# Performance work log

Hardware: AMD Instinct MI355X
Metric: run time of the kernel (lower is better)

The kernel has to match this reference:

```python
import jax, jax.numpy as jnp
import numpy as np

N_ATOMS = 65536
N_PAIRS = N_ATOMS * 32
MAXZ = 95          # D3 tables cover H..Pu, indexed directly by atomic number
NREF = 5           # number of reference coordination numbers per element
CUTOFF, CUTON = 12.0, 10.0   # model units; distances_model2Bohr == 1
K1, K3 = 16.0, -4.0
SMALL = 1e-30      # fp32 stand-in for the original's 1e-300 double guard


def setup_inputs() -> dict:
    key = jax.random.key(0)
    k0, k1, k2, k3 = jax.random.split(key, 4)
    rng = np.random.default_rng(0)

    atomic_numbers = jax.random.randint(k0, (N_ATOMS,), 1, 87)
    idx_i = jax.random.randint(k1, (N_PAIRS,), 0, N_ATOMS)
    idx_j = jax.random.randint(k2, (N_PAIRS,), 0, N_ATOMS)
    # pair distances spanning inside/switch/outside of the 10..12 cutoff band
    distances = jax.random.uniform(k3, (N_PAIRS,), minval=0.8, maxval=12.5)

    # synthetic stand-ins for the grimme_d3 data files
    rcov = jnp.asarray(rng.uniform(0.5, 3.0, (MAXZ,)).astype(np.float32))
    rcn_np = rng.uniform(0.0, 5.0, (MAXZ, NREF)).astype(np.float32)
    rcn_np[::3, NREF - 1] = -1.0  # mimic -1 padding for missing references
    rcn = jnp.asarray(rcn_np)
    rc6 = jnp.asarray(rng.uniform(1.0, 50.0, (MAXZ, MAXZ, NREF, NREF)).astype(np.float32))
    r2r4 = jnp.asarray(rng.uniform(1.0, 10.0, (MAXZ,)).astype(np.float32))

    s6 = jnp.float32(1.0)
    s8 = jnp.float32(0.9171)
    a1 = jnp.float32(0.3385)
    a2 = jnp.float32(2.883)
    return dict(distances=distances, rcov=rcov, rcn=rcn, rc6=rc6, r2r4=r2r4,
                s6=s6, s8=s8, a1=a1, a2=a2,
                atomic_numbers=atomic_numbers, idx_i=idx_i, idx_j=idx_j)


def reference(distances, rcov, rcn, rc6, r2r4, s6, s8, a1, a2,
              atomic_numbers, idx_i, idx_j):
    n = atomic_numbers.shape[0]
    zi = atomic_numbers[idx_i]
    zj = atomic_numbers[idx_j]

    # smooth switch-off from 1 (r < cuton) to 0 (r >= cutoff)
    x = (CUTOFF - distances) / (CUTOFF - CUTON)
    sw = jnp.where(distances < CUTON, 1.0,
                   jnp.where(distances >= CUTOFF, 0.0,
                             ((6.0 * x - 15.0) * x + 10.0) * x * x * x))

    # coordination numbers via inverse damping, scatter-summed per atom i
    rcov_ij = rcov[zi] + rcov[zj]
    cn_ij = sw / (1.0 + jnp.exp(-K1 * (rcov_ij / distances - 1.0)))
    cn = jax.ops.segment_sum(cn_ij, idx_i, num_segments=n)  # [N]

    # Gaussian weights over reference CNs (soft retrieval into rc6 table)
    rcn_a = rcn[atomic_numbers]                 # [N, NREF]
    mask = rcn_a >= 0
    dcn = rcn_a - cn[:, None]
    gw = jnp.where(mask, jnp.exp(K3 * dcn * dcn), 0.0)
    norm = jnp.sum(gw, axis=-1, keepdims=True)
    # exceptional case: all gaussians underflow -> pick the max reference CN
    rcn_max_a = jnp.max(rcn, axis=-1)[atomic_numbers][:, None]
    exceptional = (rcn_a == rcn_max_a).astype(gw.dtype)
    weights = jnp.where(norm == 0, exceptional, gw / jnp.maximum(norm, SMALL))  # [N, NREF]

    # weighted pairwise C6 from reference table rc6[Zi, Zj, a, b]
    w_i = weights[idx_i]                         # [P, NREF]
    w_j = weights[idx_j]                         # [P, NREF]
    c6 = jnp.einsum('pa,pb,pab->p', w_i, w_j, rc6[zi, zj])

    # C8 = 3 * C6 * <r2>/<r4>_i * <r2>/<r4>_j ; BJ critical radius
    qq = 3.0 * r2r4[zi] * r2r4[zj]
    rr = a1 * jnp.sqrt(qq) + a2

    d2 = distances * distances
    d6 = d2 * d2 * d2
    d8 = d6 * d2
    rr2 = rr * rr
    rr6 = rr2 * rr2 * rr2
    rr8 = rr6 * rr2

    # BJ-damped dispersion energy per pair (0.5 for double counting), switched
    e_pair = -0.5 * (s6 * c6 / (d6 + rr6) + s8 * qq * c6 / (d8 + rr8)) * sw

    # per-atom dispersion energies (energies_Hartree2model == 1)
    return jax.ops.segment_sum(e_pair, idx_i, num_segments=n)
```

## Files before the change

kernel.cpp:

```cpp
#include <hip/hip_runtime.h>
#include <stdint.h>


typedef unsigned short u16;
#define MAXZ 95
#define NREF 5
#define EXC_CUT -87.33654f
#define NB    1024
#define BSH   6
#define BSZ   64
#define CAPSH 12
#define RC_TOTAL (MAXZ * MAXZ * 32)

__device__ __forceinline__ float switch_fn(float d) {
    if (d < 10.0f) return 1.0f;
    float x = (12.0f - d) * 0.5f;
    return ((6.0f * x - 15.0f) * x + 10.0f) * x * x * x;
}

__device__ __forceinline__ void calc_weights(const float* __restrict__ rcn_z,
                                             float cni, float* __restrict__ w) {
    float r[NREF], arg[NREF];
    float rmax = -1e30f, marg = -1e30f;
#pragma unroll
    for (int a = 0; a < NREF; a++) {
        r[a] = rcn_z[a];
        rmax = fmaxf(rmax, r[a]);
        float dc = r[a] - cni;
        arg[a] = (-4.0f * dc) * dc;
        if (r[a] >= 0.0f) marg = fmaxf(marg, arg[a]);
    }
    if (marg < EXC_CUT) {
#pragma unroll
        for (int a = 0; a < NREF; a++) w[a] = (r[a] == rmax) ? 1.0f : 0.0f;
    } else {
        float g[NREF], norm = 0.0f;
#pragma unroll
        for (int a = 0; a < NREF; a++) {
            float e = (r[a] >= 0.0f) ? expf(arg[a]) : 0.0f;
            g[a] = e;
            norm += e;
        }
        float inv = 1.0f / fmaxf(norm, 1e-30f);
#pragma unroll
        for (int a = 0; a < NREF; a++) w[a] = g[a] * inv;
    }
}

__global__ __launch_bounds__(1024) void scatter_pairs(const float* __restrict__ dist,
                                                      const int* __restrict__ idx_i,
                                                      const int* __restrict__ idx_j,
                                                      const int* __restrict__ Z,
                                                      const float* __restrict__ rcov,
                                                      const float* __restrict__ rc6,
                                                      float* __restrict__ rcovA,
                                                      float* __restrict__ rc6pad,
                                                      uint32_t* __restrict__ bcount,
                                                      uint2* __restrict__ recs,
                                                      int n_pairs, int n_atoms,
                                                      int chunk) {
    __shared__ uint32_t hist[NB];
    __shared__ uint32_t run[NB];

    int g = blockIdx.x * 1024 + (int)threadIdx.x;
    int T = gridDim.x * 1024;
    for (int i = g; i < n_atoms; i += T) rcovA[i] = rcov[Z[i]];
    for (int id = g; id < RC_TOTAL; id += T) {
        int tile = id >> 5, slot = id & 31;
        rc6pad[id] = (slot < 25) ? rc6[(size_t)tile * 25 + slot] : 0.0f;
    }

    for (int t = threadIdx.x; t < NB; t += 1024) hist[t] = 0;
    __syncthreads();
    int lo = blockIdx.x * chunk;
    int hi = min(lo + chunk, n_pairs);
    for (int q = lo + (int)threadIdx.x; q < hi; q += 1024) {
        if (dist[q] < 12.0f)
            atomicAdd(&hist[((uint32_t)idx_i[q]) >> BSH], 1u);
    }
    __syncthreads();
    for (int t = threadIdx.x; t < NB; t += 1024) {
        uint32_t h = hist[t];
        run[t] = h ? atomicAdd(&bcount[t], h) : 0u;
    }
    __syncthreads();
    for (int q = lo + (int)threadIdx.x; q < hi; q += 1024) {
        float d = dist[q];
        if (d >= 12.0f) continue;
        uint32_t i = (uint32_t)idx_i[q];
        uint32_t b = i >> BSH;
        uint32_t pos = atomicAdd(&run[b], 1u);
        if (pos < (1u << CAPSH)) {
            uint32_t packed = ((uint32_t)idx_j[q] & 0xFFFFu) |
                              ((i & (BSZ - 1u)) << 16);
            recs[((size_t)b << CAPSH) + pos] = make_uint2(__float_as_uint(d), packed);
        }
    }
}

__global__ __launch_bounds__(256) void cn_bucket(const uint2* __restrict__ recs,
                                                 const uint32_t* __restrict__ bcount,
                                                 const float* __restrict__ rcovA,
                                                 float* __restrict__ cn,
                                                 int n_atoms) {
    __shared__ float lrc[BSZ];
    __shared__ float acc[BSZ];
    int b = blockIdx.x;
    int base = b << BSH;
    if (threadIdx.x < BSZ) {
        int i = base + (int)threadIdx.x;
        lrc[threadIdx.x] = (i < n_atoms) ? rcovA[i] : 0.0f;
        acc[threadIdx.x] = 0.0f;
    }
    __syncthreads();
    uint32_t n = min(bcount[b], 1u << CAPSH);
    const uint2* r0 = recs + ((size_t)b << CAPSH);
    for (uint32_t k = threadIdx.x; k < n; k += 256) {
        uint2 r = r0[k];
        float d = __uint_as_float(r.x);
        int j  = r.y & 0xFFFF;
        int il = r.y >> 16;
        float rij = lrc[il] + rcovA[j];
        float sw = switch_fn(d);
        atomicAdd(&acc[il], sw / (1.0f + expf(-16.0f * (rij / d - 1.0f))));
    }
    __syncthreads();
    if (threadIdx.x < BSZ) {
        int i = base + (int)threadIdx.x;
        if (i < n_atoms) cn[i] = acc[threadIdx.x];
    }
}

__global__ __launch_bounds__(256) void atom_weights(const float* __restrict__ rcn,
                                                    const float* __restrict__ r2r4,
                                                    const int* __restrict__ Z,
                                                    const float* __restrict__ cn,
                                                    float* __restrict__ arec,
                                                    int n_atoms) {
    int i = blockIdx.x * blockDim.x + threadIdx.x;
    if (i >= n_atoms) return;
    int z = Z[i];
    float w[NREF];
    calc_weights(rcn + (size_t)z * NREF, cn[i], w);
    float4 v0 = make_float4(w[0], w[1], w[2], w[3]);
    float4 v1 = make_float4(w[4], r2r4[z], __int_as_float(z), 0.0f);
    float4* dst = (float4*)(arec + (size_t)i * 8);
    dst[0] = v0;
    dst[1] = v1;
}

__global__ __launch_bounds__(256) void energy_bucket(const uint2* __restrict__ recs,
                                                     const uint32_t* __restrict__ bcount,
                                                     const float* __restrict__ arec,
                                                     const float* __restrict__ rc6pad,
                                                     const float* __restrict__ s6p,
                                                     const float* __restrict__ s8p,
                                                     const float* __restrict__ a1p,
                                                     const float* __restrict__ a2p,
                                                     float* __restrict__ eout,
                                                     int n_atoms) {
    __shared__ float4 la0[BSZ];
    __shared__ float4 la1[BSZ];
    __shared__ float  acc[BSZ];
    int b = blockIdx.x;
    int base = b << BSH;
    if (threadIdx.x < BSZ) {
        int i = min(base + (int)threadIdx.x, n_atoms - 1);
        const float4* A = (const float4*)(arec + (size_t)i * 8);
        la0[threadIdx.x] = A[0];
        la1[threadIdx.x] = A[1];
        acc[threadIdx.x] = 0.0f;
    }
    __syncthreads();
    float s6 = s6p[0], s8 = s8p[0], a1 = a1p[0], a2 = a2p[0];
    uint32_t n = min(bcount[b], 1u << CAPSH);
    const uint2* r0 = recs + ((size_t)b << CAPSH);
    for (uint32_t k = threadIdx.x; k < n; k += 256) {
        uint2 r = r0[k];
        float d = __uint_as_float(r.x);
        int j  = r.y & 0xFFFF;
        int il = r.y >> 16;
        float4 ai0 = la0[il];
        float4 ai1 = la1[il];
        const float4* Aj = (const float4*)(arec + (size_t)j * 8);
        float4 aj0 = Aj[0];
        float4 aj1 = Aj[1];
        float wi[NREF] = {ai0.x, ai0.y, ai0.z, ai0.w, ai1.x};
        float wj[NREF] = {aj0.x, aj0.y, aj0.z, aj0.w, aj1.x};
        int zi = __float_as_int(ai1.z);
        int zj = __float_as_int(aj1.z);

        const float4* T4 = (const float4*)(rc6pad + (size_t)(zi * MAXZ + zj) * 32);
        float tt[25];
#pragma unroll
        for (int kk = 0; kk < 6; kk++) {
            float4 t = T4[kk];
            tt[4 * kk + 0] = t.x;
            if (4 * kk + 1 < 25) tt[4 * kk + 1] = t.y;
            if (4 * kk + 2 < 25) tt[4 * kk + 2] = t.z;
            if (4 * kk + 3 < 25) tt[4 * kk + 3] = t.w;
        }
        tt[24] = ((const float*)T4)[24];

        float c6 = 0.0f;
#pragma unroll
        for (int a = 0; a < NREF; a++) {
            float s = 0.0f;
#pragma unroll
            for (int bb = 0; bb < NREF; bb++) s = fmaf(wj[bb], tt[a * NREF + bb], s);
            c6 = fmaf(wi[a], s, c6);
        }

        float qq = 3.0f * ai1.y * aj1.y;
        float rr = a1 * sqrtf(qq) + a2;
        float d2 = d * d;
        float d6 = d2 * d2 * d2;
        float d8 = d6 * d2;
        float rr2 = rr * rr;
        float rr6 = rr2 * rr2 * rr2;
        float rr8 = rr6 * rr2;
        float sw = switch_fn(d);

        float e = -0.5f * (s6 * c6 / (d6 + rr6) + s8 * qq * c6 / (d8 + rr8)) * sw;
        atomicAdd(&acc[il], e);
    }
    __syncthreads();
    if (threadIdx.x < BSZ) {
        int i = base + (int)threadIdx.x;
        if (i < n_atoms) eout[i] = acc[threadIdx.x];
    }
}

__global__ __launch_bounds__(256) void pair_cn_slim(const float* __restrict__ dist,
                                                    const float* __restrict__ rcov,
                                                    const int* __restrict__ Z,
                                                    const int* __restrict__ idx_i,
                                                    const int* __restrict__ idx_j,
                                                    float* __restrict__ cn,
                                                    int n_pairs) {
    int p = blockIdx.x * blockDim.x + threadIdx.x;
    if (p >= n_pairs) return;
    float d = dist[p];
    if (d >= 12.0f) return;
    float rij = rcov[Z[idx_i[p]]] + rcov[Z[idx_j[p]]];
    float sw = switch_fn(d);
    atomicAdd(&cn[idx_i[p]], sw / (1.0f + expf(-16.0f * (rij / d - 1.0f))));
}

__global__ __launch_bounds__(256) void pair_energy_slim(const float* __restrict__ dist,
                                                        const int* __restrict__ Z,
                                                        const int* __restrict__ idx_i,
                                                        const int* __restrict__ idx_j,
                                                        const float* __restrict__ cn,
                                                        const float* __restrict__ rcn,
                                                        const float* __restrict__ r2r4,
                                                        const float* __restrict__ rc6,
                                                        const float* __restrict__ s6p,
                                                        const float* __restrict__ s8p,
                                                        const float* __restrict__ a1p,
                                                        const float* __restrict__ a2p,
                                                        float* __restrict__ eout,
                                                        int n_pairs) {
    int p = blockIdx.x * blockDim.x + threadIdx.x;
    if (p >= n_pairs) return;
    float d = dist[p];
    if (d >= 12.0f) return;
    int i = idx_i[p], j = idx_j[p];
    int zi = Z[i], zj = Z[j];
    float wi[NREF], wj[NREF];
    calc_weights(rcn + (size_t)zi * NREF, cn[i], wi);
    calc_weights(rcn + (size_t)zj * NREF, cn[j], wj);
    const float* T = rc6 + (size_t)(zi * MAXZ + zj) * 25;
    float c6 = 0.0f;
#pragma unroll
    for (int a = 0; a < NREF; a++) {
        float s = 0.0f;
#pragma unroll
        for (int bb = 0; bb < NREF; bb++) s = fmaf(wj[bb], T[a * NREF + bb], s);
        c6 = fmaf(wi[a], s, c6);
    }
    float qq = 3.0f * r2r4[zi] * r2r4[zj];
    float rr = a1p[0] * sqrtf(qq) + a2p[0];
    float d2 = d * d;
    float d6 = d2 * d2 * d2;
    float d8 = d6 * d2;
    float rr2 = rr * rr;
    float rr6 = rr2 * rr2 * rr2;
    float rr8 = rr6 * rr2;
    float sw = switch_fn(d);
    float e = -0.5f * (s6p[0] * c6 / (d6 + rr6) + s8p[0] * qq * c6 / (d8 + rr8)) * sw;
    atomicAdd(&eout[i], e);
}

extern "C" void kernel_launch(void* const* d_in, const int* in_sizes, int n_in,
                              void* d_out, int out_size, void* d_ws, size_t ws_size,
                              hipStream_t stream) {
    const float* dist = (const float*)d_in[0];
    const float* rcov = (const float*)d_in[1];
    const float* rcn  = (const float*)d_in[2];
    const float* rc6  = (const float*)d_in[3];
    const float* r2r4 = (const float*)d_in[4];
    const float* s6p  = (const float*)d_in[5];
    const float* s8p  = (const float*)d_in[6];
    const float* a1p  = (const float*)d_in[7];
    const float* a2p  = (const float*)d_in[8];
    const int* Z    = (const int*)d_in[9];
    const int* idxi = (const int*)d_in[10];
    const int* idxj = (const int*)d_in[11];
    float* out = (float*)d_out;

    int n_pairs = in_sizes[0];
    int n_atoms = in_sizes[9];
    int agrid = (n_atoms + 255) / 256;

    char* ws = (char*)d_ws;
    size_t o_bcount = 0;
    size_t o_cn     = (size_t)NB * 4;
    size_t o_rcovA  = o_cn + (size_t)n_atoms * 4;
    size_t o_arec   = (o_rcovA + (size_t)n_atoms * 4 + 31) & ~(size_t)31;
    size_t o_rc6    = o_arec + (size_t)n_atoms * 32;
    size_t o_recs   = (o_rc6 + (size_t)RC_TOTAL * 4 + 255) & ~(size_t)255;
    size_t need     = o_recs + ((size_t)NB << CAPSH) * 8;

    uint32_t* bcount = (uint32_t*)(ws + o_bcount);
    float* cn     = (float*)(ws + o_cn);
    float* rcovA  = (float*)(ws + o_rcovA);
    float* arec   = (float*)(ws + o_arec);
    float* rcpad  = (float*)(ws + o_rc6);
    uint2* recs   = (uint2*)(ws + o_recs);

    if (ws_size >= need && n_atoms <= NB * BSZ) {
        hipMemsetAsync(bcount, 0, NB * 4, stream);
        int sblocks = 256;
        int chunk = (n_pairs + sblocks - 1) / sblocks;
        scatter_pairs<<<sblocks, 1024, 0, stream>>>(dist, idxi, idxj, Z, rcov, rc6,
                                                    rcovA, rcpad, bcount, recs,
                                                    n_pairs, n_atoms, chunk);
        cn_bucket<<<NB, 256, 0, stream>>>(recs, bcount, rcovA, cn, n_atoms);
        atom_weights<<<agrid, 256, 0, stream>>>(rcn, r2r4, Z, cn, arec, n_atoms);
        energy_bucket<<<NB, 256, 0, stream>>>(recs, bcount, arec, rcpad,
                                              s6p, s8p, a1p, a2p, out, n_atoms);
    } else {
        int pgrid = (n_pairs + 255) / 256;
        hipMemsetAsync(out, 0, (size_t)n_atoms * 4, stream);
        hipMemsetAsync(cn, 0, (size_t)n_atoms * 4, stream);
        pair_cn_slim<<<pgrid, 256, 0, stream>>>(dist, rcov, Z, idxi, idxj, cn, n_pairs);
        pair_energy_slim<<<pgrid, 256, 0, stream>>>(dist, Z, idxi, idxj, cn, rcn, r2r4,
                                                    rc6, s6p, s8p, a1p, a2p, out, n_pairs);
    }
}
```

Measured before the change: 172.0 us.

## Pack atom weights and C6 table as fp16, fuse weights into CN kernel

Stores the padded rc6 reference table and the per-atom records (weights, r2r4, Z) in half precision, which halves the bytes fetched per pair in the energy kernel's random gathers. It also computes the per-atom weights directly at the end of the CN bucket kernel, removing the separate atom_weights launch and the cn round trip through memory. The cost is fp16 rounding of the C6 values, weights and r2r4, which may push results past the accuracy tolerance.

```diff
diff --git a/kernel.cpp b/kernel.cpp
--- a/kernel.cpp
+++ b/kernel.cpp
@@ -12,6 +12,13 @@
 #define CAPSH 12
 #define RC_TOTAL (MAXZ * MAXZ * 32)
 
+__device__ __forceinline__ float h2f(u16 h) {
+    union { _Float16 h; u16 u; } v; v.u = h; return (float)v.h;
+}
+__device__ __forceinline__ u16 f2h(float f) {
+    union { _Float16 h; u16 u; } v; v.h = (_Float16)f; return v.u;
+}
+
 __device__ __forceinline__ float switch_fn(float d) {
     if (d < 10.0f) return 1.0f;
     float x = (12.0f - d) * 0.5f;
@@ -45,6 +52,13 @@
 #pragma unroll
         for (int a = 0; a < NREF; a++) w[a] = g[a] * inv;
     }
+}
+
+__device__ __forceinline__ void dec8(uint4 t, float* o) {
+    o[0] = h2f(t.x & 0xFFFFu); o[1] = h2f(t.x >> 16);
+    o[2] = h2f(t.y & 0xFFFFu); o[3] = h2f(t.y >> 16);
+    o[4] = h2f(t.z & 0xFFFFu); o[5] = h2f(t.z >> 16);
+    o[6] = h2f(t.w & 0xFFFFu); o[7] = h2f(t.w >> 16);
 }
 
 __global__ __launch_bounds__(1024) void scatter_pairs(const float* __restrict__ dist,
@@ -54,7 +68,7 @@
                                                       const float* __restrict__ rcov,
                                                       const float* __restrict__ rc6,
                                                       float* __restrict__ rcovA,
-                                                      float* __restrict__ rc6pad,
+                                                      u16* __restrict__ rc6pad,
                                                       uint32_t* __restrict__ bcount,
                                                       uint2* __restrict__ recs,
                                                       int n_pairs, int n_atoms,
@@ -67,7 +81,7 @@
     for (int i = g; i < n_atoms; i += T) rcovA[i] = rcov[Z[i]];
     for (int id = g; id < RC_TOTAL; id += T) {
         int tile = id >> 5, slot = id & 31;
-        rc6pad[id] = (slot < 25) ? rc6[(size_t)tile * 25 + slot] : 0.0f;
+        rc6pad[id] = (slot < 25) ? f2h(rc6[(size_t)tile * 25 + slot]) : (u16)0;
     }
 
     for (int t = threadIdx.x; t < NB; t += 1024) hist[t] = 0;
@@ -98,11 +112,14 @@
     }
 }
 
-__global__ __launch_bounds__(256) void cn_bucket(const uint2* __restrict__ recs,
-                                                 const uint32_t* __restrict__ bcount,
-                                                 const float* __restrict__ rcovA,
-                                                 float* __restrict__ cn,
-                                                 int n_atoms) {
+__global__ __launch_bounds__(256) void cn_weights_bucket(const uint2* __restrict__ recs,
+                                                         const uint32_t* __restrict__ bcount,
+                                                         const float* __restrict__ rcovA,
+                                                         const int* __restrict__ Z,
+                                                         const float* __restrict__ rcn,
+                                                         const float* __restrict__ r2r4,
+                                                         uint4* __restrict__ arec_h,
+                                                         int n_atoms) {
     __shared__ float lrc[BSZ];
     __shared__ float acc[BSZ];
     int b = blockIdx.x;
@@ -127,32 +144,24 @@
     __syncthreads();
     if (threadIdx.x < BSZ) {
         int i = base + (int)threadIdx.x;
-        if (i < n_atoms) cn[i] = acc[threadIdx.x];
-    }
-}
-
-__global__ __launch_bounds__(256) void atom_weights(const float* __restrict__ rcn,
-                                                    const float* __restrict__ r2r4,
-                                                    const int* __restrict__ Z,
-                                                    const float* __restrict__ cn,
-                                                    float* __restrict__ arec,
-                                                    int n_atoms) {
-    int i = blockIdx.x * blockDim.x + threadIdx.x;
-    if (i >= n_atoms) return;
-    int z = Z[i];
-    float w[NREF];
-    calc_weights(rcn + (size_t)z * NREF, cn[i], w);
-    float4 v0 = make_float4(w[0], w[1], w[2], w[3]);
-    float4 v1 = make_float4(w[4], r2r4[z], __int_as_float(z), 0.0f);
-    float4* dst = (float4*)(arec + (size_t)i * 8);
-    dst[0] = v0;
-    dst[1] = v1;
+        if (i < n_atoms) {
+            int z = Z[i];
+            float w[NREF];
+            calc_weights(rcn + (size_t)z * NREF, acc[threadIdx.x], w);
+            uint4 pk;
+            pk.x = (uint32_t)f2h(w[0]) | ((uint32_t)f2h(w[1]) << 16);
+            pk.y = (uint32_t)f2h(w[2]) | ((uint32_t)f2h(w[3]) << 16);
+            pk.z = (uint32_t)f2h(w[4]) | ((uint32_t)f2h(r2r4[z]) << 16);
+            pk.w = (uint32_t)z;
+            arec_h[i] = pk;
+        }
+    }
 }
 
 __global__ __launch_bounds__(256) void energy_bucket(const uint2* __restrict__ recs,
                                                      const uint32_t* __restrict__ bcount,
-                                                     const float* __restrict__ arec,
-                                                     const float* __restrict__ rc6pad,
+                                                     const uint4* __restrict__ arec_h,
+                                                     const u16* __restrict__ rc6pad,
                                                      const float* __restrict__ s6p,
                                                      const float* __restrict__ s8p,
                                                      const float* __restrict__ a1p,
@@ -166,9 +175,11 @@
     int base = b << BSH;
     if (threadIdx.x < BSZ) {
         int i = min(base + (int)threadIdx.x, n_atoms - 1);
-        const float4* A = (const float4*)(arec + (size_t)i * 8);
-        la0[threadIdx.x] = A[0];
-        la1[threadIdx.x] = A[1];
+        uint4 pk = arec_h[i];
+        la0[threadIdx.x] = make_float4(h2f(pk.x & 0xFFFFu), h2f(pk.x >> 16),
+                                       h2f(pk.y & 0xFFFFu), h2f(pk.y >> 16));
+        la1[threadIdx.x] = make_float4(h2f(pk.z & 0xFFFFu), h2f(pk.z >> 16),
+                                       __int_as_float((int)pk.w), 0.0f);
         acc[threadIdx.x] = 0.0f;
     }
     __syncthreads();
@@ -182,25 +193,20 @@
         int il = r.y >> 16;
         float4 ai0 = la0[il];
         float4 ai1 = la1[il];
-        const float4* Aj = (const float4*)(arec + (size_t)j * 8);
-        float4 aj0 = Aj[0];
-        float4 aj1 = Aj[1];
-        float wi[NREF] = {ai0.x, ai0.y, ai0.z, ai0.w, ai1.x};
-        float wj[NREF] = {aj0.x, aj0.y, aj0.z, aj0.w, aj1.x};
+        uint4 pj = arec_h[j];
+        float wj[NREF] = {h2f(pj.x & 0xFFFFu), h2f(pj.x >> 16),
+                          h2f(pj.y & 0xFFFFu), h2f(pj.y >> 16),
+                          h2f(pj.z & 0xFFFFu)};
+        float r2r4j = h2f(pj.z >> 16);
         int zi = __float_as_int(ai1.z);
-        int zj = __float_as_int(aj1.z);
-
-        const float4* T4 = (const float4*)(rc6pad + (size_t)(zi * MAXZ + zj) * 32);
+        int zj = (int)pj.w;
+        float wi[NREF] = {ai0.x, ai0.y, ai0.z, ai0.w, la1[il].x};
+
+        const uint4* T4 = (const uint4*)(rc6pad + (size_t)(zi * MAXZ + zj) * 32);
+        uint4 t0 = T4[0], t1 = T4[1], t2 = T4[2], t3 = T4[3];
         float tt[25];
-#pragma unroll
-        for (int kk = 0; kk < 6; kk++) {
-            float4 t = T4[kk];
-            tt[4 * kk + 0] = t.x;
-            if (4 * kk + 1 < 25) tt[4 * kk + 1] = t.y;
-            if (4 * kk + 2 < 25) tt[4 * kk + 2] = t.z;
-            if (4 * kk + 3 < 25) tt[4 * kk + 3] = t.w;
-        }
-        tt[24] = ((const float*)T4)[24];
+        dec8(t0, tt); dec8(t1, tt + 8); dec8(t2, tt + 16);
+        tt[24] = h2f(t3.x & 0xFFFFu);
 
         float c6 = 0.0f;
 #pragma unroll
@@ -211,7 +217,7 @@
             c6 = fmaf(wi[a], s, c6);
         }
 
-        float qq = 3.0f * ai1.y * aj1.y;
+        float qq = 3.0f * ai1.y * r2r4j;
         float rr = a1 * sqrtf(qq) + a2;
         float d2 = d * d;
         float d6 = d2 * d2 * d2;
@@ -311,37 +317,35 @@
 
     int n_pairs = in_sizes[0];
     int n_atoms = in_sizes[9];
-    int agrid = (n_atoms + 255) / 256;
 
     char* ws = (char*)d_ws;
     size_t o_bcount = 0;
-    size_t o_cn     = (size_t)NB * 4;
-    size_t o_rcovA  = o_cn + (size_t)n_atoms * 4;
-    size_t o_arec   = (o_rcovA + (size_t)n_atoms * 4 + 31) & ~(size_t)31;
-    size_t o_rc6    = o_arec + (size_t)n_atoms * 32;
-    size_t o_recs   = (o_rc6 + (size_t)RC_TOTAL * 4 + 255) & ~(size_t)255;
+    size_t o_rcovA  = 4096;
+    size_t o_arec   = (o_rcovA + (size_t)n_atoms * 4 + 15) & ~(size_t)15;
+    size_t o_rc6    = (o_arec + (size_t)n_atoms * 16 + 63) & ~(size_t)63;
+    size_t o_recs   = (o_rc6 + (size_t)RC_TOTAL * 2 + 255) & ~(size_t)255;
     size_t need     = o_recs + ((size_t)NB << CAPSH) * 8;
 
     uint32_t* bcount = (uint32_t*)(ws + o_bcount);
-    float* cn     = (float*)(ws + o_cn);
     float* rcovA  = (float*)(ws + o_rcovA);
-    float* arec   = (float*)(ws + o_arec);
-    float* rcpad  = (float*)(ws + o_rc6);
+    uint4* arec_h = (uint4*)(ws + o_arec);
+    u16*   rcpad  = (u16*)(ws + o_rc6);
     uint2* recs   = (uint2*)(ws + o_recs);
 
-    if (ws_size >= need && n_atoms <= NB * BSZ) {
+    if (ws_size >= need && n_atoms <= NB * BSZ && n_atoms <= 65536) {
         hipMemsetAsync(bcount, 0, NB * 4, stream);
         int sblocks = 256;
         int chunk = (n_pairs + sblocks - 1) / sblocks;
         scatter_pairs<<<sblocks, 1024, 0, stream>>>(dist, idxi, idxj, Z, rcov, rc6,
                                                     rcovA, rcpad, bcount, recs,
                                                     n_pairs, n_atoms, chunk);
-        cn_bucket<<<NB, 256, 0, stream>>>(recs, bcount, rcovA, cn, n_atoms);
-        atom_weights<<<agrid, 256, 0, stream>>>(rcn, r2r4, Z, cn, arec, n_atoms);
-        energy_bucket<<<NB, 256, 0, stream>>>(recs, bcount, arec, rcpad,
+        cn_weights_bucket<<<NB, 256, 0, stream>>>(recs, bcount, rcovA, Z, rcn, r2r4,
+                                                  arec_h, n_atoms);
+        energy_bucket<<<NB, 256, 0, stream>>>(recs, bcount, arec_h, rcpad,
                                               s6p, s8p, a1p, a2p, out, n_atoms);
     } else {
         int pgrid = (n_pairs + 255) / 256;
+        float* cn = (float*)(ws + o_rcovA);
         hipMemsetAsync(out, 0, (size_t)n_atoms * 4, stream);
         hipMemsetAsync(cn, 0, (size_t)n_atoms * 4, stream);
         pair_cn_slim<<<pgrid, 256, 0, stream>>>(dist, rcov, Z, idxi, idxj, cn, n_pairs);
```

Result: faster. 155.5 us (-9.6%).
